# Optimization experiments

Measured on AMD Instinct MI355X. Metric: run time of the kernel, lower is better.

Reference implementation:

```python
import jax, jax.numpy as jnp
import numpy as np

G = 4   # DCNv3 default groups
K = 3   # DCNv3 kernel size
P = K * K


def layernorm(x, g, b, eps=1e-5):
    m = jnp.mean(x, axis=-1, keepdims=True)
    v = jnp.var(x, axis=-1, keepdims=True)
    return (x - m) * jax.lax.rsqrt(v + eps) * g + b


def setup_inputs():
    key = jax.random.key(0)
    ks = jax.random.split(key, 12)
    B, Cin, C, H, W = 2, 64, 64, 512, 512
    s = lambda k, shape, sc=1.0: jax.random.normal(k, shape, jnp.float32) * sc
    return {
        "x": s(ks[0], (B, Cin, H, W)),
        "conv_w": s(ks[1], (C, Cin, 3, 3), 0.05),
        "w_in": s(ks[2], (C, C), 0.1), "b_in": s(ks[3], (C,), 0.1),
        "dw_w": s(ks[4], (3, 3, 1, C), 0.1), "dw_b": s(ks[5], (C,), 0.1),
        "ln_g": jnp.ones((C,), jnp.float32), "ln_b": jnp.zeros((C,), jnp.float32),
        "w_off": s(ks[6], (C, G * P * 2), 0.02), "b_off": s(ks[7], (G * P * 2,), 0.02),
        "w_mask": s(ks[8], (C, G * P), 0.1), "b_mask": s(ks[9], (G * P,), 0.1),
        "w_out": s(ks[10], (C, C), 0.1), "b_out": s(ks[11], (C,), 0.1),
    }


def dcnv3_core(x, offset, mask):
    # x: (N,H,W,C) projected input; offset: (N,H,W,G*P*2); mask: (N,H,W,G,P) softmaxed
    N, H, W, C = x.shape
    gc = C // G
    pad = 1
    xp = jnp.pad(x, ((0, 0), (pad, pad), (pad, pad), (0, 0)))
    Hin, Win = H + 2 * pad, W + 2 * pad
    dt = x.dtype
    # reference points: centers of each 3x3 window on the padded input, normalized
    ref_x = (jnp.arange(W, dtype=dt) + 1.5) / Win  # (dil*(k-1))//2 + 0.5 = 1.5
    ref_y = (jnp.arange(H, dtype=dt) + 1.5) / Hin
    # dilation grid: kx outer, ky inner (matches torch meshgrid 'ij' ordering)
    lin = jnp.arange(K, dtype=dt) - (K - 1) // 2
    gx, gy = jnp.meshgrid(lin, lin, indexing='ij')
    grid = jnp.stack([gx / Win, gy / Hin], -1).reshape(P, 2)  # identical for all groups
    off = offset.reshape(N, H, W, G, P, 2) / jnp.array([Win, Hin], dt)  # offset_scale=1
    loc_x = ref_x[None, None, :, None, None] + grid[:, 0] + off[..., 0]  # (N,H,W,G,P)
    loc_y = ref_y[None, :, None, None, None] + grid[:, 1] + off[..., 1]
    # grid_sample(align_corners=False): pixel = loc*size - 0.5, zero padding outside
    ix = loc_x * Win - 0.5
    iy = loc_y * Hin - 0.5
    x0f = jnp.floor(ix); y0f = jnp.floor(iy)
    fx = ix - x0f; fy = iy - y0f
    x0 = x0f.astype(jnp.int32); y0 = y0f.astype(jnp.int32)
    xg = xp.reshape(N, Hin * Win, G, gc)
    n_idx = jnp.arange(N)[:, None, None, None, None]
    g_idx = jnp.arange(G)[None, None, None, :, None]

    def corner(yc, xc, cw):
        valid = (yc >= 0) & (yc < Hin) & (xc >= 0) & (xc < Win)
        idx = jnp.clip(yc, 0, Hin - 1) * Win + jnp.clip(xc, 0, Win - 1)
        v = xg[n_idx, idx, g_idx]                     # (N,H,W,G,P,gc) irregular gather
        w = cw * valid.astype(dt) * mask              # fold mask into bilinear weight
        return jnp.einsum('nhwgpc,nhwgp->nhwgc', v, w)

    out = (corner(y0, x0, (1 - fy) * (1 - fx))
           + corner(y0, x0 + 1, (1 - fy) * fx)
           + corner(y0 + 1, x0, fy * (1 - fx))
           + corner(y0 + 1, x0 + 1, fy * fx))
    return out.reshape(N, H, W, C)


def reference(x, conv_w, w_in, b_in, dw_w, dw_b, ln_g, ln_b, w_off, b_off, w_mask, b_mask, w_out, b_out):
    # stride-2 'down' conv (no bias), then channels-last ReLU
    y = jax.lax.conv_general_dilated(x, conv_w, (2, 2), ((1, 1), (1, 1)),
                                     dimension_numbers=('NCHW', 'OIHW', 'NCHW'))
    y = jax.nn.relu(jnp.transpose(y, (0, 2, 3, 1)))  # (N,H,W,C)
    N, H, W, C = y.shape
    x_proj = y @ w_in + b_in                         # DCNv3 input_proj
    # depthwise 3x3 conv + LayerNorm + GELU for the offset/mask branch
    x1 = jax.lax.conv_general_dilated(y, dw_w, (1, 1), ((1, 1), (1, 1)),
                                      dimension_numbers=('NHWC', 'HWIO', 'NHWC'),
                                      feature_group_count=C) + dw_b
    x1 = jax.nn.gelu(layernorm(x1, ln_g, ln_b), approximate=False)
    offset = x1 @ w_off + b_off
    m = jax.nn.softmax((x1 @ w_mask + b_mask).reshape(N, H, W, G, P), axis=-1)
    out = dcnv3_core(x_proj, offset, m) @ w_out + b_out  # output_proj
    return jnp.transpose(out, (0, 3, 1, 2))  # back to NCHW
```

## Files before the change

kernel.cpp:

```cpp
#include <hip/hip_runtime.h>
#include <hip/hip_bf16.h>
#include <math.h>

#define NB 2
#define C 64
#define H 256
#define W 256
#define HIN 512
#define WIN 512
#define CIN 64
#define G 4
#define P 9
#define GC 16
#define NPIX (NB*H*W)

typedef __attribute__((ext_vector_type(8))) __bf16 bf16x8v;
typedef __attribute__((ext_vector_type(4))) float floatx4;

#define O_WOUT   47872
#define O_BIN    51968
#define O_DWW    52032
#define O_DWB    52608
#define O_LNG    52672
#define O_LNB    52736
#define O_BOFF   52800
#define O_BMASK  52872
#define O_BOUT   52908
#define O_WFRAG  53248
#define O_WINF   71680
#define O_WCOMB  73728
#define O_Y      77824
#define O_XP     (O_Y  + 8388608)
#define O_OFFS   (O_XP + 8388608)
#define O_MASK   (O_OFFS + 9437184)

static __device__ __forceinline__ unsigned pkbf(float a, float b) {
    unsigned lo = __bfloat16_as_ushort(__float2bfloat16(a));
    unsigned hi = __bfloat16_as_ushort(__float2bfloat16(b));
    return lo | (hi << 16);
}

__global__ void k_prep(const float* __restrict__ conv_w, const float* __restrict__ w_in,
                       const float* __restrict__ b_in,
                       const float* __restrict__ dw_w, const float* __restrict__ dw_b,
                       const float* __restrict__ ln_g, const float* __restrict__ ln_b,
                       const float* __restrict__ w_off, const float* __restrict__ b_off,
                       const float* __restrict__ w_mask, const float* __restrict__ b_mask,
                       const float* __restrict__ w_out, const float* __restrict__ b_out,
                       float* __restrict__ ws)
{
    int i = blockIdx.x*256 + threadIdx.x;
    if (i < 36864) {
        int j    = i & 7;
        int lane = (i >> 3) & 63;
        int nt   = (i >> 9) & 3;
        int ks   = (i >> 11) & 1;
        int tap  = i >> 12;
        int kh = tap / 3, kw = tap % 3;
        int ci = ks*32 + (lane >> 4)*8 + j;
        int co = nt*16 + (lane & 15);
        ((__hip_bfloat16*)(ws + O_WFRAG))[i] =
            __float2bfloat16(conv_w[co*576 + ci*9 + kh*3 + kw]);
    }
    if (i < 4096) {
        int j    = i & 7;
        int lane = (i >> 3) & 63;
        int s    = i >> 9;
        int nt   = s & 3, ks = s >> 2;
        int ci = ks*32 + (lane >> 4)*8 + j;
        int co = nt*16 + (lane & 15);
        ((__hip_bfloat16*)(ws + O_WINF))[i] = __float2bfloat16(w_in[ci*64 + co]);
    }
    if (i < 7168) {
        int j    = i & 7;
        int lane = (i >> 3) & 63;
        int s    = i >> 9;
        int nt   = s % 7, ks = s / 7;
        int ci = ks*32 + (lane >> 4)*8 + j;
        int jj = nt*16 + (lane & 15);
        float v = (jj < 72) ? w_off[ci*72 + jj] : (jj < 108 ? w_mask[ci*36 + (jj-72)] : 0.f);
        ((__hip_bfloat16*)(ws + O_WCOMB))[i] = __float2bfloat16(v);
    }
    if (i < 4096) ws[O_WOUT + i] = w_out[i];
    if (i < 64)   ws[O_BIN  + i] = b_in[i];
    if (i < 576)  ws[O_DWW  + i] = dw_w[i];
    if (i < 64)   ws[O_DWB  + i] = dw_b[i];
    if (i < 64)   ws[O_LNG  + i] = ln_g[i];
    if (i < 64)   ws[O_LNB  + i] = ln_b[i];
    if (i < 72)   ws[O_BOFF + i] = b_off[i];
    if (i < 36)   ws[O_BMASK+ i] = b_mask[i];
    if (i < 64)   ws[O_BOUT + i] = b_out[i];
}

__global__ __launch_bounds__(256) void k_xt(
    const float* __restrict__ x, __hip_bfloat16* __restrict__ xt)
{
    __shared__ float tile[64][65];
    int t = threadIdx.x;
    int b = blockIdx.x;
    int n  = b >> 12;
    int p0 = (b & 4095) * 64;
    const float* xb = x + (size_t)n*CIN*262144 + p0;
    #pragma unroll
    for (int k=0;k<4;k++) {
        int ch = k*16 + (t>>4);
        int p4 = (t&15)*4;
        float4 v = *(const float4*)(xb + (size_t)ch*262144 + p4);
        tile[p4+0][ch] = v.x;
        tile[p4+1][ch] = v.y;
        tile[p4+2][ch] = v.z;
        tile[p4+3][ch] = v.w;
    }
    __syncthreads();
    #pragma unroll
    for (int k=0;k<2;k++) {
        int e = k*256 + t;
        int px = e >> 3;
        int c8 = (e & 7)*8;
        __hip_bfloat16 v[8];
        #pragma unroll
        for (int j=0;j<8;j++) v[j] = __float2bfloat16(tile[px][c8+j]);
        *(uint4*)(xt + ((size_t)(n*262144 + p0 + px))*64 + c8) = *(uint4*)v;
    }
}

__global__ __launch_bounds__(256) void k_conv_mfma(
    const __hip_bfloat16* __restrict__ xt, const float* __restrict__ ws,
    float* __restrict__ y)
{
    const __hip_bfloat16* wf = (const __hip_bfloat16*)(ws + O_WFRAG);
    int t = threadIdx.x, lane = t & 63, wv = t >> 6;
    int bid = blockIdx.x;
    int nbk = (bid & 7) * (gridDim.x >> 3) + (bid >> 3);
    int pix0 = nbk*64 + wv*16;
    int n = pix0 >> 16;
    int hw = pix0 & 65535;
    int h = hw >> 8, wo0 = hw & 255;
    int m = lane & 15, q = lane >> 4;
    floatx4 acc[4] = {};
    #pragma unroll
    for (int kh=0; kh<3; kh++) {
        int ih = 2*h + kh - 1;
        if (ih < 0) continue;
        size_t rowbase = ((size_t)(n*512 + ih))*512;
        #pragma unroll
        for (int kw=0; kw<3; kw++) {
            int iw = 2*wo0 + kw - 1 + 2*m;
            bool inval = iw < 0;
            int iwc = inval ? 0 : iw;
            const __hip_bfloat16* ap = xt + (rowbase + iwc)*64 + q*8;
            const __hip_bfloat16* bp = wf + (kh*3 + kw)*4096 + lane*8;
            #pragma unroll
            for (int ks=0; ks<2; ks++) {
                uint4 au = *(const uint4*)(ap + ks*32);
                if (inval) au = make_uint4(0,0,0,0);
                bf16x8v av = __builtin_bit_cast(bf16x8v, au);
                #pragma unroll
                for (int nt=0; nt<4; nt++) {
                    uint4 bu = *(const uint4*)(bp + ks*2048 + nt*512);
                    bf16x8v bv = __builtin_bit_cast(bf16x8v, bu);
                    acc[nt] = __builtin_amdgcn_mfma_f32_16x16x32_bf16(av, bv, acc[nt], 0,0,0);
                }
            }
        }
    }
    int co0 = lane & 15;
    #pragma unroll
    for (int nt=0; nt<4; nt++)
        #pragma unroll
        for (int r=0; r<4; r++)
            y[((size_t)(pix0 + q*4 + r))*64 + nt*16 + co0] = fmaxf(acc[nt][r], 0.f);
}

__global__ __launch_bounds__(256) void k_branch(
    const float* __restrict__ y, const float* __restrict__ ws,
    float* __restrict__ offs, float* __restrict__ mask, float* __restrict__ xp)
{
    __shared__ float scr[64][68];
    __shared__ __align__(16) __hip_bfloat16 x1b[64][72];
    __shared__ __align__(16) __hip_bfloat16 ysb[64][72];
    int t = threadIdx.x;
    int lane = t & 63;
    int wv = t >> 6;
    int bid = blockIdx.x;
    int nbk = (bid & 7) * (gridDim.x >> 3) + (bid >> 3);
    int pix0 = nbk * 64;
    int n  = pix0 >> 16;
    int hw = pix0 & 65535;
    int hh = hw >> 8, ww0 = hw & 255;
    float dwv[9];
    #pragma unroll
    for (int k=0;k<9;k++) dwv[k] = ws[O_DWW + k*C + lane];
    float dbb = ws[O_DWB + lane];
    const float* ybase = y + (size_t)(n*H)*W*C + lane;
    #pragma unroll
    for (int rg=0; rg<4; rg++) {
        int i0 = wv*16 + rg*4;
        int cb = ww0 + i0 - 1;
        float cc[3][6];
        #pragma unroll
        for (int kh=0; kh<3; kh++) {
            int yh = hh + kh - 1;
            bool rv = (yh >= 0) && (yh < H);
            const float* yr = ybase + (size_t)(rv ? yh : 0)*W*C;
            #pragma unroll
            for (int c=0; c<6; c++) {
                int col = cb + c;
                bool ok = rv && (col >= 0) && (col < W);
                cc[kh][c] = ok ? yr[(ptrdiff_t)col*C] : 0.f;
            }
        }
        float a[4];
        #pragma unroll
        for (int u=0; u<4; u++) a[u] = dbb;
        #pragma unroll
        for (int kh=0; kh<3; kh++)
            #pragma unroll
            for (int kw=0; kw<3; kw++) {
                float wg = dwv[kh*3+kw];
                #pragma unroll
                for (int u=0; u<4; u++) a[u] = fmaf(cc[kh][u+kw], wg, a[u]);
            }
        #pragma unroll
        for (int u=0; u<4; u++) {
            scr[i0+u][lane] = a[u];
            ysb[i0+u][lane] = __float2bfloat16(cc[1][u+1]);
        }
    }
    asm volatile("" ::: "memory");
    {
        int pxl = lane >> 2;
        int cq  = lane & 3;
        int i   = wv*16 + pxl;
        const float* ar = &scr[i][cq*16];
        float4 V0 = *(const float4*)(ar);
        float4 V1 = *(const float4*)(ar + 4);
        float4 V2 = *(const float4*)(ar + 8);
        float4 V3 = *(const float4*)(ar + 12);
        float v[16] = {V0.x,V0.y,V0.z,V0.w, V1.x,V1.y,V1.z,V1.w,
                       V2.x,V2.y,V2.z,V2.w, V3.x,V3.y,V3.z,V3.w};
        float s = 0.f, s2 = 0.f;
        #pragma unroll
        for (int k=0;k<16;k++) { s += v[k]; s2 = fmaf(v[k], v[k], s2); }
        s  += __shfl_xor(s,  1, 64);  s  += __shfl_xor(s,  2, 64);
        s2 += __shfl_xor(s2, 1, 64);  s2 += __shfl_xor(s2, 2, 64);
        float mean = s * 0.015625f;
        float var  = fmaxf(fmaf(-mean, mean, s2 * 0.015625f), 0.f);
        float rsig = rsqrtf(var + 1e-5f);
        const float* gp = ws + O_LNG + cq*16;
        const float* bp = ws + O_LNB + cq*16;
        float4 Ga = *(const float4*)gp,      Gb = *(const float4*)(gp+4);
        float4 Gc = *(const float4*)(gp+8),  Gd = *(const float4*)(gp+12);
        float4 Ba = *(const float4*)bp,      Bb = *(const float4*)(bp+4);
        float4 Bc = *(const float4*)(bp+8),  Bd = *(const float4*)(bp+12);
        float gv[16] = {Ga.x,Ga.y,Ga.z,Ga.w, Gb.x,Gb.y,Gb.z,Gb.w,
                        Gc.x,Gc.y,Gc.z,Gc.w, Gd.x,Gd.y,Gd.z,Gd.w};
        float bv[16] = {Ba.x,Ba.y,Ba.z,Ba.w, Bb.x,Bb.y,Bb.z,Bb.w,
                        Bc.x,Bc.y,Bc.z,Bc.w, Bd.x,Bd.y,Bd.z,Bd.w};
        float gl[16];
        #pragma unroll
        for (int k=0;k<16;k++) {
            float xh = fmaf((v[k]-mean)*rsig, gv[k], bv[k]);
            gl[k] = 0.5f * xh * (1.f + erff(xh * 0.70710678118654752f));
        }
        uint4 w0, w1;
        w0.x = pkbf(gl[0],gl[1]);  w0.y = pkbf(gl[2],gl[3]);
        w0.z = pkbf(gl[4],gl[5]);  w0.w = pkbf(gl[6],gl[7]);
        w1.x = pkbf(gl[8],gl[9]);  w1.y = pkbf(gl[10],gl[11]);
        w1.z = pkbf(gl[12],gl[13]);w1.w = pkbf(gl[14],gl[15]);
        *(uint4*)&x1b[i][cq*16]     = w0;
        *(uint4*)&x1b[i][cq*16 + 8] = w1;
    }
    asm volatile("" ::: "memory");
    int m = lane & 15, q = lane >> 4;
    bf16x8v af[2];
    #pragma unroll
    for (int ks=0; ks<2; ks++)
        af[ks] = __builtin_bit_cast(bf16x8v, *(const uint4*)&x1b[wv*16 + m][ks*32 + q*8]);
    const __hip_bfloat16* wcomb = (const __hip_bfloat16*)(ws + O_WCOMB);
    #pragma unroll
    for (int nt=0; nt<7; nt++) {
        int j = nt*16 + m;
        float b = (j < 72) ? ws[O_BOFF + j] : (j < 108 ? ws[O_BMASK + j - 72] : 0.f);
        floatx4 acc = {b,b,b,b};
        #pragma unroll
        for (int ks=0; ks<2; ks++) {
            uint4 bu = *(const uint4*)(wcomb + (ks*7 + nt)*512 + lane*8);
            bf16x8v bvv = __builtin_bit_cast(bf16x8v, bu);
            acc = __builtin_amdgcn_mfma_f32_16x16x32_bf16(af[ks], bvv, acc, 0,0,0);
        }
        if (j < 72) {
            #pragma unroll
            for (int r=0;r<4;r++)
                offs[(size_t)(pix0 + wv*16 + q*4 + r)*72 + j] = acc[r];
        } else if (j < 108) {
            int jj = j - 72;
            int gg = jj / 9, qq = jj - gg*9;
            #pragma unroll
            for (int r=0;r<4;r++)
                scr[wv*16 + q*4 + r][gg*12 + qq] = acc[r];
        }
    }
    {
        const __hip_bfloat16* wfin = (const __hip_bfloat16*)(ws + O_WINF);
        bf16x8v af2[2];
        #pragma unroll
        for (int ks=0; ks<2; ks++) {
            uint4 u = *(const uint4*)&ysb[wv*16 + m][ks*32 + q*8];
            af2[ks] = __builtin_bit_cast(bf16x8v, u);
        }
        #pragma unroll
        for (int nt=0; nt<4; nt++) {
            float b = ws[O_BIN + nt*16 + m];
            floatx4 a2 = {b,b,b,b};
            #pragma unroll
            for (int ks=0; ks<2; ks++) {
                uint4 bu = *(const uint4*)(wfin + (ks*4 + nt)*512 + lane*8);
                bf16x8v bvv = __builtin_bit_cast(bf16x8v, bu);
                a2 = __builtin_amdgcn_mfma_f32_16x16x32_bf16(af2[ks], bvv, a2, 0,0,0);
            }
            #pragma unroll
            for (int r=0;r<4;r++)
                xp[((size_t)(pix0 + wv*16 + q*4 + r))*64 + nt*16 + m] = a2[r];
        }
    }
    asm volatile("" ::: "memory");
    {
        int pxl = lane >> 2;
        int i   = wv*16 + pxl;
        int g   = lane & 3;
        const float* lrow = &scr[i][g*12];
        float l[9];
        #pragma unroll
        for (int qq=0;qq<9;qq++) l[qq] = lrow[qq];
        float mx = l[0];
        #pragma unroll
        for (int qq=1;qq<9;qq++) mx = fmaxf(mx, l[qq]);
        float e[9]; float sum = 0.f;
        #pragma unroll
        for (int qq=0;qq<9;qq++) { e[qq] = expf(l[qq]-mx); sum += e[qq]; }
        float rs = 1.f / sum;
        float* mp = mask + (size_t)(pix0 + i)*36 + g*9;
        #pragma unroll
        for (int qq=0;qq<9;qq++) mp[qq] = e[qq] * rs;
    }
}

#define DPX 16
__global__ __launch_bounds__(256, 4) void k_dcn(
    const float* __restrict__ xp, const float* __restrict__ offs,
    const float* __restrict__ mask, const float* __restrict__ ws,
    float* __restrict__ out)
{
    __shared__ float core[DPX][68];
    __shared__ float ot[64][17];
    __shared__ __align__(16) float offsl[DPX*72];
    __shared__ __align__(16) float maskl[DPX*36];
    __shared__ __align__(16) float wsl[4096];
    int t = threadIdx.x;
    int lane = t & 63;
    int wv = t >> 6;
    int bid = blockIdx.x;
    int nbk = (bid & 7) * (gridDim.x >> 3) + (bid >> 3);
    int pix0 = nbk * DPX;
    {
        const float4* osrc = (const float4*)(offs + (size_t)pix0*72);
        float4* odst = (float4*)offsl;
        odst[t] = osrc[t];
        if (t < 32) odst[256 + t] = osrc[256 + t];
        const float4* msrc = (const float4*)(mask + (size_t)pix0*36);
        float4* mdst = (float4*)maskl;
        if (t < 144) mdst[t] = msrc[t];
        const float4* wsrc = (const float4*)(ws + O_WOUT);
        float4* wdst = (float4*)wsl;
        #pragma unroll
        for (int k=0;k<4;k++) wdst[k*256 + t] = wsrc[k*256 + t];
    }
    __syncthreads();
    int c4  = lane & 3;
    int g   = (lane >> 2) & 3;
    int sub = lane >> 4;
    int i   = wv*4 + sub;
    int pix = pix0 + i;
    int n  = pix >> 16;
    int hw = pix & 65535;
    int hh = hw >> 8, ww = hw & 255;
    const float* ob  = offsl + i*72 + g*18;
    const float* mb  = maskl + i*36 + g*9;
    const float* xpb = xp + (size_t)n*H*W*C + g*GC + c4*4;
    int   eo[P][4];
    float wv4[P][4];
    #pragma unroll
    for (int p=0;p<P;p++) {
        const int kx = p/3, ky = p%3;
        float offx = ob[p*2], offy = ob[p*2+1];
        float mm = mb[p];
        float ix = (float)(ww + kx) + offx;
        float iy = (float)(hh + ky) + offy;
        float x0f = floorf(ix), y0f = floorf(iy);
        float fx = ix - x0f, fy = iy - y0f;
        int x0 = (int)x0f - 1, y0 = (int)y0f - 1;
        int x1 = x0 + 1,       y1 = y0 + 1;
        bool vx0 = (x0 >= 0) & (x0 < W), vx1 = (x1 >= 0) & (x1 < W);
        bool vy0 = (y0 >= 0) & (y0 < H), vy1 = (y1 >= 0) & (y1 < H);
        int cx0 = min(max(x0,0), W-1), cx1 = min(max(x1,0), W-1);
        int ry0 = min(max(y0,0), H-1) * W, ry1 = min(max(y1,0), H-1) * W;
        float am = (1.f - fy) * mm, bm = fy * mm;
        float fxc = 1.f - fx;
        eo[p][0] = (ry0 + cx0) * C;  wv4[p][0] = (vy0 & vx0) ? am * fxc : 0.f;
        eo[p][1] = (ry0 + cx1) * C;  wv4[p][1] = (vy0 & vx1) ? am * fx  : 0.f;
        eo[p][2] = (ry1 + cx0) * C;  wv4[p][2] = (vy1 & vx0) ? bm * fxc : 0.f;
        eo[p][3] = (ry1 + cx1) * C;  wv4[p][3] = (vy1 & vx1) ? bm * fx  : 0.f;
    }
    floatx4 ac0 = {0.f,0.f,0.f,0.f}, ac1 = {0.f,0.f,0.f,0.f};
    #pragma unroll
    for (int p=0;p<P;p++) {
        float4 v0 = *(const float4*)(xpb + eo[p][0]);
        float4 v1 = *(const float4*)(xpb + eo[p][1]);
        float4 v2 = *(const float4*)(xpb + eo[p][2]);
        float4 v3 = *(const float4*)(xpb + eo[p][3]);
        float w0 = wv4[p][0], w1 = wv4[p][1], w2 = wv4[p][2], w3 = wv4[p][3];
        ac0[0] = fmaf(v0.x, w0, fmaf(v1.x, w1, ac0[0]));
        ac0[1] = fmaf(v0.y, w0, fmaf(v1.y, w1, ac0[1]));
        ac0[2] = fmaf(v0.z, w0, fmaf(v1.z, w1, ac0[2]));
        ac0[3] = fmaf(v0.w, w0, fmaf(v1.w, w1, ac0[3]));
        ac1[0] = fmaf(v2.x, w2, fmaf(v3.x, w3, ac1[0]));
        ac1[1] = fmaf(v2.y, w2, fmaf(v3.y, w3, ac1[1]));
        ac1[2] = fmaf(v2.z, w2, fmaf(v3.z, w3, ac1[2]));
        ac1[3] = fmaf(v2.w, w2, fmaf(v3.w, w3, ac1[3]));
    }
    float4 acc;
    acc.x = ac0[0] + ac1[0];
    acc.y = ac0[1] + ac1[1];
    acc.z = ac0[2] + ac1[2];
    acc.w = ac0[3] + ac1[3];
    *(float4*)&core[i][g*GC + c4*4] = acc;
    __syncthreads();
    {
        int cq = t & 15, px = t >> 4;
        float4 a = *(const float4*)(ws + O_BOUT + cq*4);
        #pragma unroll 4
        for (int c=0;c<64;c+=4) {
            float4 cv = *(const float4*)&core[px][c];
            const float* wp = wsl + c*64 + cq*4;
            float4 w0 = *(const float4*)(wp);
            float4 w1 = *(const float4*)(wp + 64);
            float4 w2 = *(const float4*)(wp + 128);
            float4 w3 = *(const float4*)(wp + 192);
            a.x += cv.x*w0.x + cv.y*w1.x + cv.z*w2.x + cv.w*w3.x;
            a.y += cv.x*w0.y + cv.y*w1.y + cv.z*w2.y + cv.w*w3.y;
            a.z += cv.x*w0.z + cv.y*w1.z + cv.z*w2.z + cv.w*w3.z;
            a.w += cv.x*w0.w + cv.y*w1.w + cv.z*w2.w + cv.w*w3.w;
        }
        ot[cq*4+0][px] = a.x;
        ot[cq*4+1][px] = a.y;
        ot[cq*4+2][px] = a.z;
        ot[cq*4+3][px] = a.w;
    }
    __syncthreads();
    {
        int n2 = pix0 >> 16, hw0 = pix0 & 65535;
        float* ob2 = out + (size_t)n2*C*65536 + hw0;
        #pragma unroll
        for (int k=0;k<4;k++) {
            int e = k*256 + t;
            int co = e >> 4, ppx = e & 15;
            ob2[(size_t)co*65536 + ppx] = ot[co][ppx];
        }
    }
}

extern "C" void kernel_launch(void* const* d_in, const int* in_sizes, int n_in,
                              void* d_out, int out_size, void* d_ws, size_t ws_size,
                              hipStream_t stream)
{
    const float* x     = (const float*)d_in[0];
    const float* convw = (const float*)d_in[1];
    const float* w_in  = (const float*)d_in[2];
    const float* b_in  = (const float*)d_in[3];
    const float* dw_w  = (const float*)d_in[4];
    const float* dw_b  = (const float*)d_in[5];
    const float* ln_g  = (const float*)d_in[6];
    const float* ln_b  = (const float*)d_in[7];
    const float* w_off = (const float*)d_in[8];
    const float* b_off = (const float*)d_in[9];
    const float* w_mask= (const float*)d_in[10];
    const float* b_mask= (const float*)d_in[11];
    const float* w_out = (const float*)d_in[12];
    const float* b_out = (const float*)d_in[13];

    float* ws   = (float*)d_ws;
    float* y    = ws + O_Y;
    float* xp   = ws + O_XP;
    float* offs = ws + O_OFFS;
    float* mask = ws + O_MASK;
    __hip_bfloat16* xt = (__hip_bfloat16*)(ws + O_XP);

    k_prep<<<144, 256, 0, stream>>>(convw, w_in, b_in, dw_w, dw_b, ln_g, ln_b,
                                    w_off, b_off, w_mask, b_mask, w_out, b_out, ws);
    k_xt<<<8192, 256, 0, stream>>>(x, xt);
    k_conv_mfma<<<2048, 256, 0, stream>>>(xt, ws, y);
    k_branch<<<NPIX/64, 256, 0, stream>>>(y, ws, offs, mask, xp);
    k_dcn<<<NPIX/DPX, 256, 0, stream>>>(xp, offs, mask, ws, (float*)d_out);
}
```

Before: 360.0 us.

## Compute DCN output projection with split-bf16 MFMA instead of fp32 FMA

Replaces the scalar fp32 output projection in k_dcn with bf16 MFMA 16x16x32 instructions, splitting both activations and weights into high and low bf16 parts (three MFMAs per k-step) to keep near-fp32 accuracy. Weights are pre-split into MFMA fragment layout in the workspace, so the 16KB per-block LDS copy of w_out and the transpose tile are removed, which frees LDS and may allow higher occupancy. Each wave then writes its output directly as float4 per channel, dropping a barrier. The accuracy of the split approximation, and any mismatch between the MFMA output layout and the store pattern, are the risks.

```diff
diff --git a/kernel.cpp b/kernel.cpp
--- a/kernel.cpp
+++ b/kernel.cpp
@@ -71,6 +71,18 @@
         int co = nt*16 + (lane & 15);
         ((__hip_bfloat16*)(ws + O_WINF))[i] = __float2bfloat16(w_in[ci*64 + co]);
     }
+    if (i < 4096) {
+        int j    = i & 7;
+        int lane = (i >> 3) & 63;
+        int s    = i >> 9;
+        int nt   = s & 3, ks = s >> 2;
+        int ci = ks*32 + (lane >> 4)*8 + j;
+        int co = nt*16 + (lane & 15);
+        float w = w_out[ci*64 + co];
+        __hip_bfloat16 h = __float2bfloat16(w);
+        ((__hip_bfloat16*)(ws + O_WOUT))[i]        = h;
+        ((__hip_bfloat16*)(ws + O_WOUT))[4096 + i] = __float2bfloat16(w - __bfloat162float(h));
+    }
     if (i < 7168) {
         int j    = i & 7;
         int lane = (i >> 3) & 63;
@@ -81,7 +93,6 @@
         float v = (jj < 72) ? w_off[ci*72 + jj] : (jj < 108 ? w_mask[ci*36 + (jj-72)] : 0.f);
         ((__hip_bfloat16*)(ws + O_WCOMB))[i] = __float2bfloat16(v);
     }
-    if (i < 4096) ws[O_WOUT + i] = w_out[i];
     if (i < 64)   ws[O_BIN  + i] = b_in[i];
     if (i < 576)  ws[O_DWW  + i] = dw_w[i];
     if (i < 64)   ws[O_DWB  + i] = dw_b[i];
@@ -353,10 +364,8 @@
     float* __restrict__ out)
 {
     __shared__ float core[DPX][68];
-    __shared__ float ot[64][17];
     __shared__ __align__(16) float offsl[DPX*72];
     __shared__ __align__(16) float maskl[DPX*36];
-    __shared__ __align__(16) float wsl[4096];
     int t = threadIdx.x;
     int lane = t & 63;
     int wv = t >> 6;
@@ -371,10 +380,6 @@
         const float4* msrc = (const float4*)(mask + (size_t)pix0*36);
         float4* mdst = (float4*)maskl;
         if (t < 144) mdst[t] = msrc[t];
-        const float4* wsrc = (const float4*)(ws + O_WOUT);
-        float4* wdst = (float4*)wsl;
-        #pragma unroll
-        for (int k=0;k<4;k++) wdst[k*256 + t] = wsrc[k*256 + t];
     }
     __syncthreads();
     int c4  = lane & 3;
@@ -437,36 +442,46 @@
     *(float4*)&core[i][g*GC + c4*4] = acc;
     __syncthreads();
     {
-        int cq = t & 15, px = t >> 4;
-        float4 a = *(const float4*)(ws + O_BOUT + cq*4);
-        #pragma unroll 4
-        for (int c=0;c<64;c+=4) {
-            float4 cv = *(const float4*)&core[px][c];
-            const float* wp = wsl + c*64 + cq*4;
-            float4 w0 = *(const float4*)(wp);
-            float4 w1 = *(const float4*)(wp + 64);
-            float4 w2 = *(const float4*)(wp + 128);
-            float4 w3 = *(const float4*)(wp + 192);
-            a.x += cv.x*w0.x + cv.y*w1.x + cv.z*w2.x + cv.w*w3.x;
-            a.y += cv.x*w0.y + cv.y*w1.y + cv.z*w2.y + cv.w*w3.y;
-            a.z += cv.x*w0.z + cv.y*w1.z + cv.z*w2.z + cv.w*w3.z;
-            a.w += cv.x*w0.w + cv.y*w1.w + cv.z*w2.w + cv.w*w3.w;
-        }
-        ot[cq*4+0][px] = a.x;
-        ot[cq*4+1][px] = a.y;
-        ot[cq*4+2][px] = a.z;
-        ot[cq*4+3][px] = a.w;
-    }
-    __syncthreads();
-    {
+        int m = lane & 15, q = lane >> 4;
+        bf16x8v ah[2], al[2];
+        #pragma unroll
+        for (int ks=0; ks<2; ks++) {
+            const float* ar = &core[m][ks*32 + q*8];
+            float4 A0 = *(const float4*)ar;
+            float4 A1 = *(const float4*)(ar + 4);
+            float av[8] = {A0.x,A0.y,A0.z,A0.w, A1.x,A1.y,A1.z,A1.w};
+            float rv[8];
+            #pragma unroll
+            for (int j=0;j<8;j++) {
+                __hip_bfloat16 hb = __float2bfloat16(av[j]);
+                rv[j] = av[j] - __bfloat162float(hb);
+            }
+            uint4 uh, ul;
+            uh.x = pkbf(av[0],av[1]); uh.y = pkbf(av[2],av[3]);
+            uh.z = pkbf(av[4],av[5]); uh.w = pkbf(av[6],av[7]);
+            ul.x = pkbf(rv[0],rv[1]); ul.y = pkbf(rv[2],rv[3]);
+            ul.z = pkbf(rv[4],rv[5]); ul.w = pkbf(rv[6],rv[7]);
+            ah[ks] = __builtin_bit_cast(bf16x8v, uh);
+            al[ks] = __builtin_bit_cast(bf16x8v, ul);
+        }
+        const __hip_bfloat16* wof = (const __hip_bfloat16*)(ws + O_WOUT);
+        floatx4 a = {0.f,0.f,0.f,0.f};
+        #pragma unroll
+        for (int ks=0; ks<2; ks++) {
+            uint4 bhu = *(const uint4*)(wof + (ks*4 + wv)*512 + lane*8);
+            uint4 blu = *(const uint4*)(wof + 4096 + (ks*4 + wv)*512 + lane*8);
+            bf16x8v bh = __builtin_bit_cast(bf16x8v, bhu);
+            bf16x8v bl = __builtin_bit_cast(bf16x8v, blu);
+            a = __builtin_amdgcn_mfma_f32_16x16x32_bf16(ah[ks], bh, a, 0,0,0);
+            a = __builtin_amdgcn_mfma_f32_16x16x32_bf16(ah[ks], bl, a, 0,0,0);
+            a = __builtin_amdgcn_mfma_f32_16x16x32_bf16(al[ks], bh, a, 0,0,0);
+        }
+        int co = wv*16 + m;
+        float bo = ws[O_BOUT + co];
         int n2 = pix0 >> 16, hw0 = pix0 & 65535;
-        float* ob2 = out + (size_t)n2*C*65536 + hw0;
-        #pragma unroll
-        for (int k=0;k<4;k++) {
-            int e = k*256 + t;
-            int co = e >> 4, ppx = e & 15;
-            ob2[(size_t)co*65536 + ppx] = ot[co][ppx];
-        }
+        float4 st;
+        st.x = a[0] + bo; st.y = a[1] + bo; st.z = a[2] + bo; st.w = a[3] + bo;
+        *(float4*)(out + (size_t)n2*C*65536 + (size_t)co*65536 + hw0 + q*4) = st;
     }
 }
 
```

Result: faster. 351.0 us (-2.5%).
